# Kernel tuning notes

Measured on AMD Instinct MI355X. Metric: run time of the kernel, lower is better.

## Reference

```python
import jax, jax.numpy as jnp
import numpy as np

NH = 32          # num_attention_heads
LAYER_ID = 3     # -> query_key_layer_scaling_coeff = 4.0
ROPE_BASE = 10000.0


def setup_inputs() -> dict:
    key = jax.random.key(0)
    k1, k2, k3, k4, k5 = jax.random.split(key, 5)
    S, B, H = 2048, 1, 4096
    hidden_states = jax.random.normal(k1, (S, B, H), dtype=jnp.float32)
    position_ids = jnp.broadcast_to(jnp.arange(S, dtype=jnp.int64)[None, :], (B, S))
    # causal mask: True means masked out (torch masked_fill semantics)
    mask = jnp.triu(jnp.ones((S, S), dtype=bool), k=1)[None, None, :, :]
    qkv_w = jax.random.normal(k2, (3 * H, H), dtype=jnp.float32) * 0.02
    qkv_b = jax.random.normal(k3, (3 * H,), dtype=jnp.float32) * 0.02
    dense_w = jax.random.normal(k4, (H, H), dtype=jnp.float32) * 0.02
    dense_b = jax.random.normal(k5, (H,), dtype=jnp.float32) * 0.02
    return {"hidden_states": hidden_states, "position_ids": position_ids, "mask": mask,
            "qkv_w": qkv_w, "qkv_b": qkv_b, "dense_w": dense_w, "dense_b": dense_b}


def _rotate_half(x):
    h = x.shape[-1] // 2
    return jnp.concatenate((-x[..., h:], x[..., :h]), axis=-1)


def reference(hidden_states, position_ids, mask, qkv_w, qkv_b, dense_w, dense_b):
    S, B, H = hidden_states.shape
    nh = NH
    hd = H // nh
    coeff = float(LAYER_ID + 1)

    # fused QKV projection: [S, B, 3H] -> [S, B, nh, 3*hd] -> split
    mixed = hidden_states @ qkv_w.T + qkv_b
    mixed = mixed.reshape(S, B, nh, 3 * hd)
    q, k, v = jnp.split(mixed, 3, axis=-1)  # each [S, B, nh, hd]

    # rotary embedding indexed by position_ids (transposed to [S, B])
    pos = position_ids.T  # [S, B]
    inv_freq = 1.0 / (ROPE_BASE ** (jnp.arange(0, hd, 2, dtype=jnp.float32) / hd))
    freqs = pos.astype(jnp.float32)[..., None] * inv_freq  # [S, B, hd/2]
    emb = jnp.concatenate((freqs, freqs), axis=-1)          # [S, B, hd]
    cos = jnp.cos(emb)[:, :, None, :]                       # [S, B, 1, hd]
    sin = jnp.sin(emb)[:, :, None, :]
    q = q * cos + _rotate_half(q) * sin
    k = k * cos + _rotate_half(k) * sin

    # scaled attention scores with per-layer coefficient
    q = q / (jnp.sqrt(jnp.float32(hd)) * coeff)
    scores = jnp.einsum('sbnh,tbnh->bnst', q, k)            # [B, nh, S, S]
    scores = jnp.where(mask, jnp.float32(-10000.0), scores)
    probs = jax.nn.softmax(scores.astype(jnp.float32) * coeff, axis=-1)
    probs = probs.astype(scores.dtype)

    context = jnp.einsum('bnst,tbnh->sbnh', probs, v).reshape(S, B, H)
    output = context @ dense_w.T + dense_b                  # [S, B, H]
    return output
```

## Files before the change

kernel.cpp:

```cpp
#include <hip/hip_runtime.h>
#include <hip/hip_bf16.h>
#include <cstdint>

#define SQ   2048
#define HIDD 4096
#define NH_  32
#define HD_  128

typedef __attribute__((ext_vector_type(8))) __bf16 bf16x8;
typedef __attribute__((ext_vector_type(4))) float  f32x4;

__device__ __forceinline__ unsigned short f2bf(float f) {
  union { float f; unsigned u; } v; v.f = f;
  return (unsigned short)((v.u + 0x7FFFu + ((v.u >> 16) & 1u)) >> 16);
}
__device__ __forceinline__ float bf2f(unsigned short u) {
  union { unsigned u; float f; } v; v.u = ((unsigned)u) << 16; return v.f;
}
__device__ __forceinline__ void gload16(const void* g, void* l) {
  __builtin_amdgcn_global_load_lds((const __attribute__((address_space(1))) void*)g,
                                   (__attribute__((address_space(3))) void*)l, 16, 0, 0);
}
#define BAR()   asm volatile("s_barrier" ::: "memory")
#define VMC(N)  asm volatile("s_waitcnt vmcnt(" #N ")" ::: "memory")
#define MFMA_(a, b, c) __builtin_amdgcn_mfma_f32_16x16x32_bf16(a, b, c, 0, 0, 0)

__global__ __launch_bounds__(256) void k_conv2(const float* __restrict__ s0,
                                               unsigned short* __restrict__ d0, int n0,
                                               const float* __restrict__ s1,
                                               unsigned short* __restrict__ d1, int n1) {
  int i = blockIdx.x * blockDim.x + threadIdx.x;
  int stride = gridDim.x * blockDim.x;
  int total = n0 + n1;
  for (; i < total; i += stride) {
    const float4* sp; ushort4* dp; int j;
    if (i < n0) { sp = (const float4*)s0; dp = (ushort4*)d0; j = i; }
    else        { sp = (const float4*)s1; dp = (ushort4*)d1; j = i - n0; }
    float4 f = sp[j];
    ushort4 o;
    o.x = f2bf(f.x); o.y = f2bf(f.y); o.z = f2bf(f.z); o.w = f2bf(f.w);
    dp[j] = o;
  }
}

__global__ __launch_bounds__(256) void k_conv(const float* __restrict__ src,
                                              unsigned short* __restrict__ dst, int n4) {
  int i = blockIdx.x * blockDim.x + threadIdx.x;
  int stride = gridDim.x * blockDim.x;
  for (; i < n4; i += stride) {
    float4 f = ((const float4*)src)[i];
    ushort4 o;
    o.x = f2bf(f.x); o.y = f2bf(f.y); o.z = f2bf(f.z); o.w = f2bf(f.w);
    ((ushort4*)dst)[i] = o;
  }
}

template<int MODE, int BN_>
__global__ __launch_bounds__(256, 2)
void k_gemm3(const unsigned short* __restrict__ A, const unsigned short* __restrict__ B,
             const float* __restrict__ bias, float* __restrict__ outf,
             unsigned short* __restrict__ qb, unsigned short* __restrict__ kb,
             unsigned short* __restrict__ vb, int K) {
  constexpr int NS   = 4 + BN_ / 32;
  constexpr int NF   = BN_ / 64;
  constexpr int BUFB = 16384 + BN_ * 128;
  __shared__ __align__(16) char lds[2 * BUFB];
  const int t = threadIdx.x;
  const int lane = t & 63, wc = t >> 6;
  const int lr = lane & 15, lg = lane >> 4;
  const int gx = gridDim.x;
  const int nwg = gx * gridDim.y;
  const int id = blockIdx.y * gx + blockIdx.x;
  const int cpx = nwg >> 3;
  const int swz = (id & 7) * cpx + (id >> 3);
  const int bm = swz % gx, bn = swz / gx;

  const unsigned short* src[NS];
  int dst[NS];
#pragma unroll
  for (int j = 0; j < NS; ++j) {
    int o = j * 4096 + t * 16;
    dst[j] = o;
    if (o < 16384) {
      int row = o >> 7, colb = o & 127;
      src[j] = A + (size_t)(bm * 128 + row) * K + ((colb ^ ((row & 7) << 4)) >> 1);
    } else {
      int o2 = o - 16384;
      int row = o2 >> 7, colb = o2 & 127;
      src[j] = B + (size_t)(bn * BN_ + row) * K + ((colb ^ ((row & 7) << 4)) >> 1);
    }
  }

  f32x4 acc[8][NF] = {};
  const int nk = K >> 6;
  const int swA = (lr & 7) << 4;

#pragma unroll
  for (int j = 0; j < NS; ++j) gload16(src[j], lds + dst[j]);

  int c = 0;
  for (int kt = 0; kt < nk; ++kt) {
    char* const bufc = lds + c * BUFB;
    char* const bufn = lds + (c ^ 1) * BUFB;
    if (kt + 1 < nk) {
      const int koff = (kt + 1) * 64;
#pragma unroll
      for (int j = 0; j < NS; ++j) gload16(src[j] + koff, bufn + dst[j]);
      if constexpr (NS == 10) VMC(10); else VMC(8);
    } else {
      VMC(0);
    }
    BAR();

    bf16x8 bfr[NF][2];
#pragma unroll
    for (int n = 0; n < NF; ++n) {
      const char* base = bufc + 16384 + (wc * (BN_ / 4) + n * 16 + lr) * 128;
#pragma unroll
      for (int kk = 0; kk < 2; ++kk)
        bfr[n][kk] = *(const bf16x8*)(base + ((kk * 64 + lg * 16) ^ swA));
    }
    __builtin_amdgcn_s_setprio(1);
#pragma unroll
    for (int m = 0; m < 8; ++m) {
      const char* abase = bufc + (m * 16 + lr) * 128;
      bf16x8 a0 = *(const bf16x8*)(abase + ((lg * 16) ^ swA));
      bf16x8 a1 = *(const bf16x8*)(abase + ((64 + lg * 16) ^ swA));
#pragma unroll
      for (int n = 0; n < NF; ++n) {
        acc[m][n] = MFMA_(a0, bfr[n][0], acc[m][n]);
        acc[m][n] = MFMA_(a1, bfr[n][1], acc[m][n]);
      }
    }
    __builtin_amdgcn_s_setprio(0);
    BAR();
    c ^= 1;
  }

#pragma unroll
  for (int m = 0; m < 8; ++m) {
    int row0 = bm * 128 + m * 16 + lg * 4;
#pragma unroll
    for (int n = 0; n < NF; ++n) {
      int col = bn * BN_ + wc * (BN_ / 4) + n * 16 + lr;
      float bv = bias[col];
      if (MODE == 0) {
        int h = col / 384, rem = col - h * 384;
        int sel = rem >> 7, d = rem & 127;
        unsigned short* dstp = sel == 0 ? qb : (sel == 1 ? kb : vb);
#pragma unroll
        for (int r = 0; r < 4; ++r)
          dstp[((size_t)h * SQ + row0 + r) * HD_ + d] = f2bf(acc[m][n][r] + bv);
      } else {
#pragma unroll
        for (int r = 0; r < 4; ++r)
          outf[(size_t)(row0 + r) * HIDD + col] = acc[m][n][r] + bv;
      }
    }
  }
}

__global__ __launch_bounds__(256) void k_rope(unsigned short* __restrict__ q,
                                              unsigned short* __restrict__ k) {
  int idx = blockIdx.x * blockDim.x + threadIdx.x;
  int i = idx & 63;
  int s = (idx >> 6) & (SQ - 1);
  int h = idx >> 17;
  float inv = __expf(-(float)i * (9.210340371976184f / 64.0f));
  float f = (float)s * inv;
  float sn, cs;
  sincosf(f, &sn, &cs);
  size_t base = ((size_t)h * SQ + s) * HD_ + i;
  const float qs = 0.08838834764831845f;
  float q0 = bf2f(q[base]), q1 = bf2f(q[base + 64]);
  q[base]      = f2bf((q0 * cs - q1 * sn) * qs);
  q[base + 64] = f2bf((q1 * cs + q0 * sn) * qs);
  float k0 = bf2f(k[base]), k1 = bf2f(k[base + 64]);
  k[base]      = f2bf(k0 * cs - k1 * sn);
  k[base + 64] = f2bf(k1 * cs + k0 * sn);
}

__global__ __launch_bounds__(256) void k_trans(const unsigned short* __restrict__ v,
                                               unsigned short* __restrict__ vt) {
  __shared__ unsigned short tile[32][33];
  const int h = blockIdx.z;
  const int sb = blockIdx.x * 32, db = blockIdx.y * 32;
  const unsigned short* src = v + (size_t)h * SQ * HD_;
  unsigned short* dst = vt + (size_t)h * HD_ * SQ;
  for (int r = threadIdx.y; r < 32; r += 8)
    tile[r][threadIdx.x] = src[(size_t)(sb + r) * HD_ + db + threadIdx.x];
  __syncthreads();
  for (int r = threadIdx.y; r < 32; r += 8)
    dst[(size_t)(db + r) * SQ + sb + threadIdx.x] = tile[threadIdx.x][r];
}

__global__ __launch_bounds__(256)
void k_attn(const unsigned short* __restrict__ q, const unsigned short* __restrict__ k,
            const unsigned short* __restrict__ vt, unsigned short* __restrict__ ctx) {
  __shared__ __align__(16) unsigned short Ks[2][64 * 128];
  __shared__ __align__(16) unsigned short Vs[2][128 * 64];
  __shared__ __align__(16) unsigned short Ps[4][16 * 64];

  const int h = blockIdx.y;
  const int t = threadIdx.x;
  const int lane = t & 63, wv = t >> 6;
  const int lr = lane & 15, lg = lane >> 4;

  const unsigned short* Kg = k + (size_t)h * SQ * HD_;
  const unsigned short* Vg = vt + (size_t)h * HD_ * SQ;
  char* const pb = (char*)(Ps[wv]);

  auto stage = [&](int kv0, int b) {
#pragma unroll
    for (int it = 0; it < 4; ++it) {
      int o = it * 4096 + t * 16;
      int krow = o >> 8, kcb = o & 255;
      int kscb = kcb ^ ((krow & 7) << 4);
      gload16(Kg + (size_t)(kv0 + krow) * HD_ + (kscb >> 1), (char*)Ks[b] + o);
      int vrow = o >> 7, vcb = o & 127;
      int vscb = vcb ^ ((vrow & 7) << 4);
      gload16(Vg + (size_t)vrow * SQ + kv0 + (vscb >> 1), (char*)Vs[b] + o);
    }
  };

  for (int ph = 0; ph < 2; ++ph) {
    const int tph = (ph == 0) ? (int)blockIdx.x : 31 - (int)blockIdx.x;
    const int q0p = tph * 64;
    const int qrow = wv * 16 + lg * 4;

    const unsigned short* Q = q + ((size_t)h * SQ + q0p + wv * 16) * HD_;
    bf16x8 qf[4];
#pragma unroll
    for (int kk = 0; kk < 4; ++kk)
      qf[kk] = *(const bf16x8*)(Q + (size_t)lr * HD_ + kk * 32 + lg * 8);

    f32x4 ot[8] = {};
    float l_p[4] = {0.f, 0.f, 0.f, 0.f};

    const int nkt = tph + 1;
    stage(0, 0);
    for (int kt = 0; kt < nkt; ++kt) {
      if (kt + 1 < nkt) { stage((kt + 1) * 64, (kt + 1) & 1); VMC(8); }
      else              { VMC(0); }
      BAR();
      const char* kl = (const char*)Ks[kt & 1];
      const char* vl = (const char*)Vs[kt & 1];

      f32x4 sc[4] = {};
#pragma unroll
      for (int ct = 0; ct < 4; ++ct) {
        int row = ct * 16 + lr;
        const char* kbase = kl + row * 256;
#pragma unroll
        for (int kk = 0; kk < 4; ++kk) {
          bf16x8 kf = *(const bf16x8*)(kbase + ((kk * 64 + lg * 16) ^ ((row & 7) << 4)));
          sc[ct] = MFMA_(qf[kk], kf, sc[ct]);
        }
      }

      if (kt == tph) {
#pragma unroll
        for (int ct = 0; ct < 4; ++ct) {
          int col = ct * 16 + lr;
#pragma unroll
          for (int r = 0; r < 4; ++r)
            if (col > qrow + r) sc[ct][r] = -1e30f;
        }
      }

      float pr[4][4];
#pragma unroll
      for (int ct = 0; ct < 4; ++ct)
#pragma unroll
        for (int r = 0; r < 4; ++r) {
          pr[ct][r] = __expf(sc[ct][r]);
          l_p[r] += pr[ct][r];
        }

#pragma unroll
      for (int ct = 0; ct < 4; ++ct)
#pragma unroll
        for (int r = 0; r < 4; ++r) {
          int row = lg * 4 + r;
          int byte = row * 128 + ((ct * 32 + lr * 2) ^ ((row & 7) << 4));
          *(unsigned short*)(pb + byte) = f2bf(pr[ct][r]);
        }
      bf16x8 pa[2];
#pragma unroll
      for (int k2 = 0; k2 < 2; ++k2)
        pa[k2] = *(const bf16x8*)(pb + lr * 128 + ((k2 * 64 + lg * 16) ^ ((lr & 7) << 4)));

#pragma unroll
      for (int dt = 0; dt < 8; ++dt) {
        int row = dt * 16 + lr;
        const char* vbase = vl + row * 128;
        bf16x8 vf0 = *(const bf16x8*)(vbase + ((lg * 16) ^ ((row & 7) << 4)));
        bf16x8 vf1 = *(const bf16x8*)(vbase + ((64 + lg * 16) ^ ((row & 7) << 4)));
        ot[dt] = MFMA_(pa[0], vf0, ot[dt]);
        ot[dt] = MFMA_(pa[1], vf1, ot[dt]);
      }
      BAR();
    }

    float l_r[4];
#pragma unroll
    for (int r = 0; r < 4; ++r) {
      l_r[r] = l_p[r];
#pragma unroll
      for (int off = 1; off < 16; off <<= 1)
        l_r[r] += __shfl_xor(l_r[r], off, 64);
    }
    float inv[4];
#pragma unroll
    for (int r = 0; r < 4; ++r) inv[r] = 1.0f / l_r[r];
#pragma unroll
    for (int dt = 0; dt < 8; ++dt)
#pragma unroll
      for (int r = 0; r < 4; ++r)
        ctx[(size_t)(q0p + wv * 16 + lg * 4 + r) * HIDD + h * HD_ + dt * 16 + lr] =
            f2bf(ot[dt][r] * inv[r]);
  }
}

extern "C" void kernel_launch(void* const* d_in, const int* in_sizes, int n_in,
                              void* d_out, int out_size, void* d_ws, size_t ws_size,
                              hipStream_t stream) {
  const float* hidden  = (const float*)d_in[0];
  const float* qkv_w   = (const float*)d_in[3];
  const float* qkv_b   = (const float*)d_in[4];
  const float* dense_w = (const float*)d_in[5];
  const float* dense_b = (const float*)d_in[6];
  float* out = (float*)d_out;

  char* ws = (char*)d_ws;
  unsigned short* wbuf = (unsigned short*)ws;
  unsigned short* hidb = (unsigned short*)(ws + 100663296);
  unsigned short* vtb  = hidb;
  unsigned short* qb   = (unsigned short*)(ws + 117440512);
  unsigned short* kb   = (unsigned short*)(ws + 134217728);
  unsigned short* vb   = (unsigned short*)(ws + 150994944);
  unsigned short* ctx  = (unsigned short*)(ws + 167772160);
  if (ws_size < 184549376ull) return;

  k_conv2<<<2048, 256, 0, stream>>>(hidden, hidb, 8388608 / 4, qkv_w, wbuf, 50331648 / 4);
  k_gemm3<0, 192><<<dim3(16, 64), 256, 0, stream>>>(hidb, wbuf, qkv_b, nullptr, qb, kb, vb, 4096);
  k_rope<<<16384, 256, 0, stream>>>(qb, kb);
  k_trans<<<dim3(64, 4, 32), dim3(32, 8), 0, stream>>>(vb, vtb);
  k_attn<<<dim3(16, 32), 256, 0, stream>>>(qb, kb, vtb, ctx);
  k_conv<<<2048, 256, 0, stream>>>(dense_w, wbuf, 16777216 / 4);
  k_gemm3<1, 128><<<dim3(16, 32), 256, 0, stream>>>(ctx, wbuf, dense_b, out, nullptr, nullptr, nullptr, 4096);
}
```

Baseline: 429.6 us.

## Fuse fp32-to-bf16 weight conversion into GEMM B-tile loading

Instead of a separate pass converting the QKV and dense weights to bf16 in a workspace buffer, the GEMM now loads fp32 weight tiles into registers, converts them to bf16, and writes them swizzled into LDS. This removes the standalone conversion kernels and the bf16 weight round-trip through memory. In exchange, every M-tile block rereads fp32 weights (twice the bytes), and register pressure rises from holding the prefetched float4s. The prefetch/compute pipeline also gains an extra vmcnt/lgkmcnt wait stage.

```diff
diff --git a/kernel.cpp b/kernel.cpp
--- a/kernel.cpp
+++ b/kernel.cpp
@@ -23,24 +23,16 @@
 }
 #define BAR()   asm volatile("s_barrier" ::: "memory")
 #define VMC(N)  asm volatile("s_waitcnt vmcnt(" #N ")" ::: "memory")
+#define LGK0()  asm volatile("s_waitcnt lgkmcnt(0)" ::: "memory")
 #define MFMA_(a, b, c) __builtin_amdgcn_mfma_f32_16x16x32_bf16(a, b, c, 0, 0, 0)
 
-__global__ __launch_bounds__(256) void k_conv2(const float* __restrict__ s0,
-                                               unsigned short* __restrict__ d0, int n0,
-                                               const float* __restrict__ s1,
-                                               unsigned short* __restrict__ d1, int n1) {
-  int i = blockIdx.x * blockDim.x + threadIdx.x;
-  int stride = gridDim.x * blockDim.x;
-  int total = n0 + n1;
-  for (; i < total; i += stride) {
-    const float4* sp; ushort4* dp; int j;
-    if (i < n0) { sp = (const float4*)s0; dp = (ushort4*)d0; j = i; }
-    else        { sp = (const float4*)s1; dp = (ushort4*)d1; j = i - n0; }
-    float4 f = sp[j];
-    ushort4 o;
-    o.x = f2bf(f.x); o.y = f2bf(f.y); o.z = f2bf(f.z); o.w = f2bf(f.w);
-    dp[j] = o;
-  }
+__device__ __forceinline__ bf16x8 cvt8(float4 a, float4 b) {
+  union { bf16x8 v; __hip_bfloat162 h[4]; } u;
+  u.h[0] = __float22bfloat162_rn(float2{a.x, a.y});
+  u.h[1] = __float22bfloat162_rn(float2{a.z, a.w});
+  u.h[2] = __float22bfloat162_rn(float2{b.x, b.y});
+  u.h[3] = __float22bfloat162_rn(float2{b.z, b.w});
+  return u.v;
 }
 
 __global__ __launch_bounds__(256) void k_conv(const float* __restrict__ src,
@@ -57,11 +49,11 @@
 
 template<int MODE, int BN_>
 __global__ __launch_bounds__(256, 2)
-void k_gemm3(const unsigned short* __restrict__ A, const unsigned short* __restrict__ B,
+void k_gemmW(const unsigned short* __restrict__ A, const float* __restrict__ Bf,
              const float* __restrict__ bias, float* __restrict__ outf,
              unsigned short* __restrict__ qb, unsigned short* __restrict__ kb,
              unsigned short* __restrict__ vb, int K) {
-  constexpr int NS   = 4 + BN_ / 32;
+  constexpr int NB   = BN_ / 32;
   constexpr int NF   = BN_ / 64;
   constexpr int BUFB = 16384 + BN_ * 128;
   __shared__ __align__(16) char lds[2 * BUFB];
@@ -75,38 +67,60 @@
   const int swz = (id & 7) * cpx + (id >> 3);
   const int bm = swz % gx, bn = swz / gx;
 
-  const unsigned short* src[NS];
-  int dst[NS];
-#pragma unroll
-  for (int j = 0; j < NS; ++j) {
+  const unsigned short* srcA[4];
+  int dstA[4];
+#pragma unroll
+  for (int j = 0; j < 4; ++j) {
     int o = j * 4096 + t * 16;
-    dst[j] = o;
-    if (o < 16384) {
-      int row = o >> 7, colb = o & 127;
-      src[j] = A + (size_t)(bm * 128 + row) * K + ((colb ^ ((row & 7) << 4)) >> 1);
-    } else {
-      int o2 = o - 16384;
-      int row = o2 >> 7, colb = o2 & 127;
-      src[j] = B + (size_t)(bn * BN_ + row) * K + ((colb ^ ((row & 7) << 4)) >> 1);
-    }
+    int row = o >> 7, colb = o & 127;
+    srcA[j] = A + (size_t)(bm * 128 + row) * K + ((colb ^ ((row & 7) << 4)) >> 1);
+    dstA[j] = o;
+  }
+  const float* bsrc[NB];
+  int bdst[NB];
+#pragma unroll
+  for (int j = 0; j < NB; ++j) {
+    int o2 = j * 4096 + t * 16;
+    int row = o2 >> 7, colb = o2 & 127;
+    bsrc[j] = Bf + (size_t)(bn * BN_ + row) * K + (colb >> 1);
+    bdst[j] = 16384 + row * 128 + (colb ^ ((row & 7) << 4));
   }
 
   f32x4 acc[8][NF] = {};
   const int nk = K >> 6;
   const int swA = (lr & 7) << 4;
-
-#pragma unroll
-  for (int j = 0; j < NS; ++j) gload16(src[j], lds + dst[j]);
-
-  int c = 0;
+  float4 br[NB][2];
+
+  auto loadB = [&](int kt) {
+#pragma unroll
+    for (int j = 0; j < NB; ++j) {
+      br[j][0] = *(const float4*)(bsrc[j] + kt * 64);
+      br[j][1] = *(const float4*)(bsrc[j] + kt * 64 + 4);
+    }
+  };
+  auto loadA = [&](int kt, char* buf) {
+#pragma unroll
+    for (int j = 0; j < 4; ++j) gload16(srcA[j] + kt * 64, buf + dstA[j]);
+  };
+  auto writeB = [&](char* buf) {
+#pragma unroll
+    for (int j = 0; j < NB; ++j)
+      *(bf16x8*)(buf + bdst[j]) = cvt8(br[j][0], br[j][1]);
+  };
+
+  loadB(0);
+  loadA(0, lds);
+  VMC(4);
+  writeB(lds);
+  LGK0();
+
   for (int kt = 0; kt < nk; ++kt) {
-    char* const bufc = lds + c * BUFB;
-    char* const bufn = lds + (c ^ 1) * BUFB;
+    char* const bufc = lds + (kt & 1) * BUFB;
+    char* const bufn = lds + ((kt + 1) & 1) * BUFB;
     if (kt + 1 < nk) {
-      const int koff = (kt + 1) * 64;
-#pragma unroll
-      for (int j = 0; j < NS; ++j) gload16(src[j] + koff, bufn + dst[j]);
-      if constexpr (NS == 10) VMC(10); else VMC(8);
+      loadB(kt + 1);
+      loadA(kt + 1, bufn);
+      if constexpr (NB == 6) VMC(16); else VMC(12);
     } else {
       VMC(0);
     }
@@ -133,8 +147,13 @@
       }
     }
     __builtin_amdgcn_s_setprio(0);
+
+    if (kt + 1 < nk) {
+      VMC(4);
+      writeB(bufn);
+    }
+    LGK0();
     BAR();
-    c ^= 1;
   }
 
 #pragma unroll
@@ -333,7 +352,6 @@
   float* out = (float*)d_out;
 
   char* ws = (char*)d_ws;
-  unsigned short* wbuf = (unsigned short*)ws;
   unsigned short* hidb = (unsigned short*)(ws + 100663296);
   unsigned short* vtb  = hidb;
   unsigned short* qb   = (unsigned short*)(ws + 117440512);
@@ -342,11 +360,10 @@
   unsigned short* ctx  = (unsigned short*)(ws + 167772160);
   if (ws_size < 184549376ull) return;
 
-  k_conv2<<<2048, 256, 0, stream>>>(hidden, hidb, 8388608 / 4, qkv_w, wbuf, 50331648 / 4);
-  k_gemm3<0, 192><<<dim3(16, 64), 256, 0, stream>>>(hidb, wbuf, qkv_b, nullptr, qb, kb, vb, 4096);
+  k_conv<<<2048, 256, 0, stream>>>(hidden, hidb, 8388608 / 4);
+  k_gemmW<0, 192><<<dim3(16, 64), 256, 0, stream>>>(hidb, qkv_w, qkv_b, nullptr, qb, kb, vb, 4096);
   k_rope<<<16384, 256, 0, stream>>>(qb, kb);
   k_trans<<<dim3(64, 4, 32), dim3(32, 8), 0, stream>>>(vb, vtb);
   k_attn<<<dim3(16, 32), 256, 0, stream>>>(qb, kb, vtb, ctx);
-  k_conv<<<2048, 256, 0, stream>>>(dense_w, wbuf, 16777216 / 4);
-  k_gemm3<1, 128><<<dim3(16, 32), 256, 0, stream>>>(ctx, wbuf, dense_b, out, nullptr, nullptr, nullptr, 4096);
-}
+  k_gemmW<1, 128><<<dim3(16, 32), 256, 0, stream>>>(ctx, dense_w, dense_b, out, nullptr, nullptr, nullptr, 4096);
+}
```

Measured after the change: 513.8 us. 1.2x slower.

## Fuse V transpose into QKV GEMM epilogue and merge paired attention tiles

Applied to the files above, without the earlier changes.

The QKV GEMM epilogue now writes V directly in transposed [h][d][s] layout, which removes the separate transpose kernel and its extra read and write of V. The attention kernel no longer runs its two causal q-tiles one after the other. It processes both tiles in a single KV loop, so each staged K/V block is loaded once and shared by both tiles. In exchange, register pressure rises (two sets of accumulators), and the transposed V stores from the GEMM epilogue are strided.

```diff
diff --git a/kernel.cpp b/kernel.cpp
--- a/kernel.cpp
+++ b/kernel.cpp
@@ -60,7 +60,7 @@
 void k_gemm3(const unsigned short* __restrict__ A, const unsigned short* __restrict__ B,
              const float* __restrict__ bias, float* __restrict__ outf,
              unsigned short* __restrict__ qb, unsigned short* __restrict__ kb,
-             unsigned short* __restrict__ vb, int K) {
+             unsigned short* __restrict__ vtb, int K) {
   constexpr int NS   = 4 + BN_ / 32;
   constexpr int NF   = BN_ / 64;
   constexpr int BUFB = 16384 + BN_ * 128;
@@ -147,10 +147,16 @@
       if (MODE == 0) {
         int h = col / 384, rem = col - h * 384;
         int sel = rem >> 7, d = rem & 127;
-        unsigned short* dstp = sel == 0 ? qb : (sel == 1 ? kb : vb);
-#pragma unroll
-        for (int r = 0; r < 4; ++r)
-          dstp[((size_t)h * SQ + row0 + r) * HD_ + d] = f2bf(acc[m][n][r] + bv);
+        if (sel == 2) {
+          unsigned short* vp = vtb + ((size_t)h * HD_ + d) * SQ + row0;
+#pragma unroll
+          for (int r = 0; r < 4; ++r) vp[r] = f2bf(acc[m][n][r] + bv);
+        } else {
+          unsigned short* dstp = sel == 0 ? qb : kb;
+#pragma unroll
+          for (int r = 0; r < 4; ++r)
+            dstp[((size_t)h * SQ + row0 + r) * HD_ + d] = f2bf(acc[m][n][r] + bv);
+        }
       } else {
 #pragma unroll
         for (int r = 0; r < 4; ++r)
@@ -180,35 +186,26 @@
   k[base + 64] = f2bf(k1 * cs + k0 * sn);
 }
 
-__global__ __launch_bounds__(256) void k_trans(const unsigned short* __restrict__ v,
-                                               unsigned short* __restrict__ vt) {
-  __shared__ unsigned short tile[32][33];
-  const int h = blockIdx.z;
-  const int sb = blockIdx.x * 32, db = blockIdx.y * 32;
-  const unsigned short* src = v + (size_t)h * SQ * HD_;
-  unsigned short* dst = vt + (size_t)h * HD_ * SQ;
-  for (int r = threadIdx.y; r < 32; r += 8)
-    tile[r][threadIdx.x] = src[(size_t)(sb + r) * HD_ + db + threadIdx.x];
-  __syncthreads();
-  for (int r = threadIdx.y; r < 32; r += 8)
-    dst[(size_t)(db + r) * SQ + sb + threadIdx.x] = tile[threadIdx.x][r];
-}
-
 __global__ __launch_bounds__(256)
 void k_attn(const unsigned short* __restrict__ q, const unsigned short* __restrict__ k,
             const unsigned short* __restrict__ vt, unsigned short* __restrict__ ctx) {
   __shared__ __align__(16) unsigned short Ks[2][64 * 128];
   __shared__ __align__(16) unsigned short Vs[2][128 * 64];
-  __shared__ __align__(16) unsigned short Ps[4][16 * 64];
+  __shared__ __align__(16) unsigned short PsA[4][16 * 64];
+  __shared__ __align__(16) unsigned short PsB[4][16 * 64];
 
   const int h = blockIdx.y;
+  const int bx = blockIdx.x;
+  const int tA = 31 - bx, tB = bx;
   const int t = threadIdx.x;
   const int lane = t & 63, wv = t >> 6;
   const int lr = lane & 15, lg = lane >> 4;
+  const int qrow = wv * 16 + lg * 4;
 
   const unsigned short* Kg = k + (size_t)h * SQ * HD_;
   const unsigned short* Vg = vt + (size_t)h * HD_ * SQ;
-  char* const pb = (char*)(Ps[wv]);
+  char* const pbA = (char*)(PsA[wv]);
+  char* const pbB = (char*)(PsB[wv]);
 
   auto stage = [&](int kv0, int b) {
 #pragma unroll
@@ -223,103 +220,141 @@
     }
   };
 
-  for (int ph = 0; ph < 2; ++ph) {
-    const int tph = (ph == 0) ? (int)blockIdx.x : 31 - (int)blockIdx.x;
-    const int q0p = tph * 64;
-    const int qrow = wv * 16 + lg * 4;
-
-    const unsigned short* Q = q + ((size_t)h * SQ + q0p + wv * 16) * HD_;
-    bf16x8 qf[4];
-#pragma unroll
-    for (int kk = 0; kk < 4; ++kk)
-      qf[kk] = *(const bf16x8*)(Q + (size_t)lr * HD_ + kk * 32 + lg * 8);
-
-    f32x4 ot[8] = {};
-    float l_p[4] = {0.f, 0.f, 0.f, 0.f};
-
-    const int nkt = tph + 1;
-    stage(0, 0);
-    for (int kt = 0; kt < nkt; ++kt) {
-      if (kt + 1 < nkt) { stage((kt + 1) * 64, (kt + 1) & 1); VMC(8); }
-      else              { VMC(0); }
-      BAR();
-      const char* kl = (const char*)Ks[kt & 1];
-      const char* vl = (const char*)Vs[kt & 1];
-
-      f32x4 sc[4] = {};
+  const unsigned short* QA = q + ((size_t)h * SQ + tA * 64 + wv * 16) * HD_;
+  const unsigned short* QB = q + ((size_t)h * SQ + tB * 64 + wv * 16) * HD_;
+  bf16x8 qfA[4], qfB[4];
+#pragma unroll
+  for (int kk = 0; kk < 4; ++kk) {
+    qfA[kk] = *(const bf16x8*)(QA + (size_t)lr * HD_ + kk * 32 + lg * 8);
+    qfB[kk] = *(const bf16x8*)(QB + (size_t)lr * HD_ + kk * 32 + lg * 8);
+  }
+
+  f32x4 otA[8] = {}, otB[8] = {};
+  float lA[4] = {0.f, 0.f, 0.f, 0.f}, lB[4] = {0.f, 0.f, 0.f, 0.f};
+
+  stage(0, 0);
+  for (int kt = 0; kt <= tA; ++kt) {
+    if (kt < tA) { stage((kt + 1) * 64, (kt + 1) & 1); VMC(8); }
+    else         { VMC(0); }
+    BAR();
+    const char* kl = (const char*)Ks[kt & 1];
+    const char* vl = (const char*)Vs[kt & 1];
+    const bool doB = (kt <= tB);
+
+    f32x4 scA[4] = {}, scB[4] = {};
+#pragma unroll
+    for (int ct = 0; ct < 4; ++ct) {
+      int row = ct * 16 + lr;
+      const char* kbase = kl + row * 256;
+#pragma unroll
+      for (int kk = 0; kk < 4; ++kk) {
+        bf16x8 kf = *(const bf16x8*)(kbase + ((kk * 64 + lg * 16) ^ ((row & 7) << 4)));
+        scA[ct] = MFMA_(qfA[kk], kf, scA[ct]);
+        if (doB) scB[ct] = MFMA_(qfB[kk], kf, scB[ct]);
+      }
+    }
+    if (kt == tA) {
 #pragma unroll
       for (int ct = 0; ct < 4; ++ct) {
-        int row = ct * 16 + lr;
-        const char* kbase = kl + row * 256;
-#pragma unroll
-        for (int kk = 0; kk < 4; ++kk) {
-          bf16x8 kf = *(const bf16x8*)(kbase + ((kk * 64 + lg * 16) ^ ((row & 7) << 4)));
-          sc[ct] = MFMA_(qf[kk], kf, sc[ct]);
-        }
-      }
-
-      if (kt == tph) {
-#pragma unroll
-        for (int ct = 0; ct < 4; ++ct) {
-          int col = ct * 16 + lr;
-#pragma unroll
-          for (int r = 0; r < 4; ++r)
-            if (col > qrow + r) sc[ct][r] = -1e30f;
-        }
-      }
-
+        int col = ct * 16 + lr;
+#pragma unroll
+        for (int r = 0; r < 4; ++r)
+          if (col > qrow + r) scA[ct][r] = -1e30f;
+      }
+    }
+    if (doB && kt == tB) {
+#pragma unroll
+      for (int ct = 0; ct < 4; ++ct) {
+        int col = ct * 16 + lr;
+#pragma unroll
+        for (int r = 0; r < 4; ++r)
+          if (col > qrow + r) scB[ct][r] = -1e30f;
+      }
+    }
+
+    {
       float pr[4][4];
 #pragma unroll
       for (int ct = 0; ct < 4; ++ct)
 #pragma unroll
         for (int r = 0; r < 4; ++r) {
-          pr[ct][r] = __expf(sc[ct][r]);
-          l_p[r] += pr[ct][r];
-        }
-
+          pr[ct][r] = __expf(scA[ct][r]);
+          lA[r] += pr[ct][r];
+        }
 #pragma unroll
       for (int ct = 0; ct < 4; ++ct)
 #pragma unroll
         for (int r = 0; r < 4; ++r) {
           int row = lg * 4 + r;
           int byte = row * 128 + ((ct * 32 + lr * 2) ^ ((row & 7) << 4));
-          *(unsigned short*)(pb + byte) = f2bf(pr[ct][r]);
-        }
-      bf16x8 pa[2];
+          *(unsigned short*)(pbA + byte) = f2bf(pr[ct][r]);
+        }
+    }
+    if (doB) {
+      float pr[4][4];
+#pragma unroll
+      for (int ct = 0; ct < 4; ++ct)
+#pragma unroll
+        for (int r = 0; r < 4; ++r) {
+          pr[ct][r] = __expf(scB[ct][r]);
+          lB[r] += pr[ct][r];
+        }
+#pragma unroll
+      for (int ct = 0; ct < 4; ++ct)
+#pragma unroll
+        for (int r = 0; r < 4; ++r) {
+          int row = lg * 4 + r;
+          int byte = row * 128 + ((ct * 32 + lr * 2) ^ ((row & 7) << 4));
+          *(unsigned short*)(pbB + byte) = f2bf(pr[ct][r]);
+        }
+    }
+    bf16x8 paA[2], paB[2] = {};
+#pragma unroll
+    for (int k2 = 0; k2 < 2; ++k2)
+      paA[k2] = *(const bf16x8*)(pbA + lr * 128 + ((k2 * 64 + lg * 16) ^ ((lr & 7) << 4)));
+    if (doB) {
 #pragma unroll
       for (int k2 = 0; k2 < 2; ++k2)
-        pa[k2] = *(const bf16x8*)(pb + lr * 128 + ((k2 * 64 + lg * 16) ^ ((lr & 7) << 4)));
-
-#pragma unroll
-      for (int dt = 0; dt < 8; ++dt) {
-        int row = dt * 16 + lr;
-        const char* vbase = vl + row * 128;
-        bf16x8 vf0 = *(const bf16x8*)(vbase + ((lg * 16) ^ ((row & 7) << 4)));
-        bf16x8 vf1 = *(const bf16x8*)(vbase + ((64 + lg * 16) ^ ((row & 7) << 4)));
-        ot[dt] = MFMA_(pa[0], vf0, ot[dt]);
-        ot[dt] = MFMA_(pa[1], vf1, ot[dt]);
-      }
-      BAR();
-    }
-
-    float l_r[4];
+        paB[k2] = *(const bf16x8*)(pbB + lr * 128 + ((k2 * 64 + lg * 16) ^ ((lr & 7) << 4)));
+    }
+
+#pragma unroll
+    for (int dt = 0; dt < 8; ++dt) {
+      int row = dt * 16 + lr;
+      const char* vbase = vl + row * 128;
+      bf16x8 vf0 = *(const bf16x8*)(vbase + ((lg * 16) ^ ((row & 7) << 4)));
+      bf16x8 vf1 = *(const bf16x8*)(vbase + ((64 + lg * 16) ^ ((row & 7) << 4)));
+      otA[dt] = MFMA_(paA[0], vf0, otA[dt]);
+      otA[dt] = MFMA_(paA[1], vf1, otA[dt]);
+      if (doB) {
+        otB[dt] = MFMA_(paB[0], vf0, otB[dt]);
+        otB[dt] = MFMA_(paB[1], vf1, otB[dt]);
+      }
+    }
+    BAR();
+  }
+
+  float invA[4], invB[4];
+#pragma unroll
+  for (int r = 0; r < 4; ++r) {
+    float a = lA[r], b = lB[r];
+#pragma unroll
+    for (int off = 1; off < 16; off <<= 1) {
+      a += __shfl_xor(a, off, 64);
+      b += __shfl_xor(b, off, 64);
+    }
+    invA[r] = 1.0f / a;
+    invB[r] = 1.0f / b;
+  }
+#pragma unroll
+  for (int dt = 0; dt < 8; ++dt)
 #pragma unroll
     for (int r = 0; r < 4; ++r) {
-      l_r[r] = l_p[r];
-#pragma unroll
-      for (int off = 1; off < 16; off <<= 1)
-        l_r[r] += __shfl_xor(l_r[r], off, 64);
-    }
-    float inv[4];
-#pragma unroll
-    for (int r = 0; r < 4; ++r) inv[r] = 1.0f / l_r[r];
-#pragma unroll
-    for (int dt = 0; dt < 8; ++dt)
-#pragma unroll
-      for (int r = 0; r < 4; ++r)
-        ctx[(size_t)(q0p + wv * 16 + lg * 4 + r) * HIDD + h * HD_ + dt * 16 + lr] =
-            f2bf(ot[dt][r] * inv[r]);
-  }
+      ctx[(size_t)(tA * 64 + qrow + r) * HIDD + h * HD_ + dt * 16 + lr] =
+          f2bf(otA[dt][r] * invA[r]);
+      ctx[(size_t)(tB * 64 + qrow + r) * HIDD + h * HD_ + dt * 16 + lr] =
+          f2bf(otB[dt][r] * invB[r]);
+    }
 }
 
 extern "C" void kernel_launch(void* const* d_in, const int* in_sizes, int n_in,
@@ -335,17 +370,15 @@
   char* ws = (char*)d_ws;
   unsigned short* wbuf = (unsigned short*)ws;
   unsigned short* hidb = (unsigned short*)(ws + 100663296);
-  unsigned short* vtb  = hidb;
   unsigned short* qb   = (unsigned short*)(ws + 117440512);
   unsigned short* kb   = (unsigned short*)(ws + 134217728);
-  unsigned short* vb   = (unsigned short*)(ws + 150994944);
+  unsigned short* vtb  = (unsigned short*)(ws + 150994944);
   unsigned short* ctx  = (unsigned short*)(ws + 167772160);
   if (ws_size < 184549376ull) return;
 
   k_conv2<<<2048, 256, 0, stream>>>(hidden, hidb, 8388608 / 4, qkv_w, wbuf, 50331648 / 4);
-  k_gemm3<0, 192><<<dim3(16, 64), 256, 0, stream>>>(hidb, wbuf, qkv_b, nullptr, qb, kb, vb, 4096);
+  k_gemm3<0, 192><<<dim3(16, 64), 256, 0, stream>>>(hidb, wbuf, qkv_b, nullptr, qb, kb, vtb, 4096);
   k_rope<<<16384, 256, 0, stream>>>(qb, kb);
-  k_trans<<<dim3(64, 4, 32), dim3(32, 8), 0, stream>>>(vb, vtb);
   k_attn<<<dim3(16, 32), 256, 0, stream>>>(qb, kb, vtb, ctx);
   k_conv<<<2048, 256, 0, stream>>>(dense_w, wbuf, 16777216 / 4);
   k_gemm3<1, 128><<<dim3(16, 32), 256, 0, stream>>>(ctx, wbuf, dense_b, out, nullptr, nullptr, nullptr, 4096);
```

New measurement: 493.4 us. 14.8% more time.
